# Optimization experiments

Measured on AMD Instinct MI355X. Metric: run time of the kernel, lower is better.

The kernel has to match this reference:

```python
import jax, jax.numpy as jnp
import numpy as np

NEG_SLOPE_GAT = 0.2    # PyG GATConv default negative_slope
NEG_SLOPE_ACT = 0.01   # F.leaky_relu default
D_DIRECTIONS = 4       # len(target): message directions per variable (uniform in this setup)
GAT_HEADS = 4


def gru_cell(x, h, Wih, Whh, bih, bhh):
    # torch.nn.GRUCell math; Wih [3H, in], Whh [3H, H]
    gi = x @ Wih.T + bih
    gh = h @ Whh.T + bhh
    ir, iz, inn = jnp.split(gi, 3, axis=1)
    hr, hz, hn = jnp.split(gh, 3, axis=1)
    r = jax.nn.sigmoid(ir + hr)
    z = jax.nn.sigmoid(iz + hz)
    n = jnp.tanh(inn + r * hn)
    return (1.0 - z) * n + z * h


def gat_conv(x, W, a_src, a_dst, bias, src, dst, heads, concat):
    # PyG GATConv (self-loops already included in src/dst)
    N = x.shape[0]
    C = W.shape[1] // heads
    h = (x @ W).reshape(N, heads, C)
    as_ = jnp.einsum('nhc,hc->nh', h, a_src)
    ad = jnp.einsum('nhc,hc->nh', h, a_dst)
    e = jax.nn.leaky_relu(as_[src] + ad[dst], NEG_SLOPE_GAT)  # [E, heads]
    m = jax.ops.segment_max(e, dst, num_segments=N)
    ex = jnp.exp(e - m[dst])
    den = jax.ops.segment_sum(ex, dst, num_segments=N)
    alpha = ex / den[dst]
    out = jax.ops.segment_sum(h[src] * alpha[:, :, None], dst, num_segments=N)
    if concat:
        return out.reshape(N, heads * C) + bias
    return out.mean(axis=1) + bias


def setup_inputs():
    key = jax.random.key(0)
    ki = iter(jax.random.split(key, 64))
    nk = lambda: next(ki)
    Nx, A, B = 100000, 50000, 50000
    IC, PD = 16, 3
    GH = IC - PD  # gru hidden = 13
    E, M, G, L, H, OC = 2000000, 1024, 1024, 4, 4, 32
    Ntot = Nx + A + B

    def p(*shape):
        return jax.random.normal(nk(), shape, jnp.float32) * 0.05

    inp = {}
    inp['x'] = jax.random.normal(nk(), (Nx, IC), jnp.float32)
    inp['edge_index'] = jax.random.randint(nk(), (2, E), 0, Ntot)
    inp['ass_to_sum_msg'] = jax.random.normal(nk(), (A, 1), jnp.float32)
    inp['ass_to_sum_hidden'] = jax.random.normal(nk(), (A, GH), jnp.float32)
    inp['sum_to_ass_msg'] = jax.random.normal(nk(), (B, 1), jnp.float32)
    inp['sum_to_ass_hidden'] = jax.random.normal(nk(), (B, GH), jnp.float32)
    inp['prefix'] = jax.random.normal(nk(), (A + B, PD), jnp.float32)
    inp['function_node_idxes'] = jax.random.randint(nk(), (M,), 0, Ntot)
    # regularized neighbor_idx_info: group g has direction idx=group_idx[g], src list group_src[g]
    # with idx at position 0 (out_i == 0) and no other entry equal to idx.
    gidx = jax.random.randint(nk(), (G,), 0, M)
    gs = jax.random.randint(nk(), (G, L), 0, M)
    rest = jnp.where(gs[:, 1:] == gidx[:, None], (gidx[:, None] + 1) % M, gs[:, 1:])
    inp['group_idx'] = gidx
    inp['group_src'] = jnp.concatenate([gidx[:, None], rest], axis=1)
    # GRU params
    for g in ('gru1', 'gru2'):
        inp[g + '_Wih'] = p(3 * GH, 1)
        inp[g + '_Whh'] = p(3 * GH, GH)
        inp[g + '_bih'] = p(3 * GH)
        inp[g + '_bhh'] = p(3 * GH)
    # GATConv params (W stored [in, heads*out], used as x @ W)
    inp['W1'] = p(IC, 32); inp['asrc1'] = p(4, 8); inp['adst1'] = p(4, 8); inp['b1'] = p(32)
    inp['W2'] = p(32, 32); inp['asrc2'] = p(4, 8); inp['adst2'] = p(4, 8); inp['b2'] = p(32)
    inp['W3'] = p(32, 32); inp['asrc3'] = p(4, 8); inp['adst3'] = p(4, 8); inp['b3'] = p(32)
    inp['W4'] = p(32, 4 * OC); inp['asrc4'] = p(4, OC); inp['adst4'] = p(4, OC); inp['b4'] = p(OC)
    # Attention heads: Wq/Wk [H, OC, OC] (applied as v @ Wq[h]), Ws [H, 2*OC], bs [H]
    inp['Wq'] = p(H, OC, OC); inp['Wk'] = p(H, OC, OC); inp['Ws'] = p(H, 2 * OC); inp['bs'] = p(H)
    return inp


def reference(x, edge_index, ass_to_sum_msg, ass_to_sum_hidden, sum_to_ass_msg,
              sum_to_ass_hidden, prefix, function_node_idxes, group_idx, group_src,
              gru1_Wih, gru1_Whh, gru1_bih, gru1_bhh,
              gru2_Wih, gru2_Whh, gru2_bih, gru2_bhh,
              W1, asrc1, adst1, b1, W2, asrc2, adst2, b2,
              W3, asrc3, adst3, b3, W4, asrc4, adst4, b4,
              Wq, Wk, Ws, bs):
    h1 = gru_cell(ass_to_sum_msg, ass_to_sum_hidden, gru1_Wih, gru1_Whh, gru1_bih, gru1_bhh)
    h2 = gru_cell(sum_to_ass_msg, sum_to_ass_hidden, gru2_Wih, gru2_Whh, gru2_bih, gru2_bhh)
    hidden = jnp.concatenate([h1, h2], axis=0)
    hidden = jnp.concatenate([prefix, hidden], axis=1)
    xx = jnp.concatenate([x, hidden], axis=0)
    N = xx.shape[0]
    loop = jnp.arange(N)
    src = jnp.concatenate([edge_index[0], loop])  # add self loops (PyG default)
    dst = jnp.concatenate([edge_index[1], loop])
    xx = jax.nn.leaky_relu(gat_conv(xx, W1, asrc1, adst1, b1, src, dst, GAT_HEADS, True), NEG_SLOPE_ACT)
    xx = jax.nn.leaky_relu(gat_conv(xx, W2, asrc2, adst2, b2, src, dst, GAT_HEADS, True), NEG_SLOPE_ACT)
    xx = jax.nn.leaky_relu(gat_conv(xx, W3, asrc3, adst3, b3, src, dst, GAT_HEADS, True), NEG_SLOPE_ACT)
    xx = jax.nn.leaky_relu(gat_conv(xx, W4, asrc4, adst4, b4, src, dst, GAT_HEADS, False), NEG_SLOPE_ACT)
    pooling = xx[function_node_idxes]  # [M, OC]
    hdim = pooling.shape[1]
    # score(i,j,h) = sigmoid((pooling_i @ Wq_h) . ws_q_h + (pooling_j @ Wk_h) . ws_k_h + bs_h)
    # (associativity: equals sigmoid(score_proj(cat([q_proj, k_proj]))) of the original)
    Vq = jnp.einsum('hdo,ho->hd', Wq, Ws[:, :hdim])
    Vk = jnp.einsum('hdo,ho->hd', Wk, Ws[:, hdim:])
    sq = pooling @ Vq.T  # [M, H]
    sk = pooling @ Vk.T  # [M, H]
    scores = jax.nn.sigmoid(sq[:, None, :] + sk[None, :, :] + bs)  # [M, M, H]; flat n -> (n//M, n%M)
    idx = group_idx
    nbr = group_src[:, 1:]  # idx itself sits at position 0 and is removed
    gathered = scores[idx[:, None], nbr]  # [G, L-1, H]
    trg = scores[idx, idx]                # [G, H]
    score_sum = gathered.mean(axis=1)
    tw = jax.nn.softmax(jnp.stack([score_sum, trg], axis=0), axis=0)  # [2, G, H]
    w = jax.nn.softmax(gathered, axis=1) * tw[0][:, None, :] * (D_DIRECTIONS - 1)
    weights = jnp.concatenate([tw[1][:, None, :], w], axis=1)  # [G, L, H] (out_i == 0)
    return weights, h1, h2
```

## Files before the change

### kernel.cpp

```cpp
#include <hip/hip_runtime.h>
#include <hip/hip_bf16.h>

#define NXD   100000
#define AROWS 50000
#define NND   200000
#define EED   2000000
#define ETOT  2200000
#define GHD   13
#define MMD   1024

#define OUT_H1 16384
#define OUT_H2 (16384 + AROWS * GHD)

#define NB    196
#define BSH   10
#define CAP   16000
#define TILE  4096

typedef __hip_bfloat16 bf16;
typedef unsigned int uvec4 __attribute__((ext_vector_type(4)));

__device__ __forceinline__ float bf2f(bf16 v) { return __bfloat162float(v); }
__device__ __forceinline__ float sigm(float x) { return 1.f / (1.f + __expf(-x)); }
__device__ __forceinline__ float tanhfast(float x) {
    x = fminf(15.f, fmaxf(-15.f, x));
    float t = __expf(-2.f * x);
    return (1.f - t) / (1.f + t);
}
__device__ __forceinline__ float lrelu(float x, float s) { return x > 0.f ? x : s * x; }

__device__ __forceinline__ unsigned short f2bf_bits(float v) {
    bf16 b = __float2bfloat16(v);
    return *reinterpret_cast<unsigned short*>(&b);
}
__device__ __forceinline__ float bflo(unsigned int u) { return __uint_as_float((u & 0xFFFFu) << 16); }
__device__ __forceinline__ float bfhi(unsigned int u) { return __uint_as_float(u & 0xFFFF0000u); }

__device__ __forceinline__ float loadF(const void* p, size_t i, int f32) {
    return f32 ? ((const float*)p)[i] : bf2f(((const bf16*)p)[i]);
}
__device__ __forceinline__ void storeF(void* p, size_t i, float v, int f32) {
    if (f32) ((float*)p)[i] = v;
    else ((bf16*)p)[i] = __float2bfloat16(v);
}

__global__ void detect_kernel(const void* __restrict__ xp, int* __restrict__ flag,
                              int* __restrict__ gtail) {
    int lane = threadIdx.x;
    const unsigned short* u = (const unsigned short*)xp;
    unsigned short b = u[lane * 2];
    int e = (b >> 7) & 0xFF;
    int viol = (e == 0xFF) || (e < 64) || (e > 190);
    unsigned long long mask = __ballot(viol != 0);
    if (lane == 0) flag[0] = (__popcll(mask) > 8) ? 1 : 0;
    for (int i = lane; i < NB; i += 64) gtail[i] = 0;
}

__global__ void assemble_kernel(const void* __restrict__ x, const void* __restrict__ prefix,
                                bf16* __restrict__ bufA, const int* __restrict__ flag) {
    int f = *flag;
    int t = blockIdx.x * 256 + threadIdx.x;
    if (t < NXD * 16) {
        bufA[t] = __float2bfloat16(loadF(x, t, f));
    } else {
        int u = t - NXD * 16;
        if (u < NXD * 3) {
            int r = u / 3, c = u - r * 3;
            bufA[(size_t)(NXD + r) * 16 + c] = __float2bfloat16(loadF(prefix, u, f));
        }
    }
}

__global__ void gru2_kernel(const void* __restrict__ msg1, const void* __restrict__ hid1,
                            const void* __restrict__ Wih1, const void* __restrict__ Whh1,
                            const void* __restrict__ bih1, const void* __restrict__ bhh1,
                            const void* __restrict__ msg2, const void* __restrict__ hid2,
                            const void* __restrict__ Wih2, const void* __restrict__ Whh2,
                            const void* __restrict__ bih2, const void* __restrict__ bhh2,
                            void* __restrict__ dout, bf16* __restrict__ xxA,
                            const int* __restrict__ flag) {
    int f = *flag;
    int which = blockIdx.x >= 196;
    const void* msg = which ? msg2 : msg1;
    const void* hid = which ? hid2 : hid1;
    const void* Wih = which ? Wih2 : Wih1;
    const void* Whh = which ? Whh2 : Whh1;
    const void* bih = which ? bih2 : bih1;
    const void* bhh = which ? bhh2 : bhh1;
    size_t houtbase = which ? (size_t)OUT_H2 : (size_t)OUT_H1;
    int rowbase = which ? AROWS : 0;
    int blk = blockIdx.x - (which ? 196 : 0);
    __shared__ float WhhL[39 * 13], WihL[39], bihL[39], bhhL[39];
    int tid = threadIdx.x;
    for (int i = tid; i < 39 * 13; i += 256) WhhL[i] = loadF(Whh, i, f);
    if (tid < 39) { WihL[tid] = loadF(Wih, tid, f); bihL[tid] = loadF(bih, tid, f); bhhL[tid] = loadF(bhh, tid, f); }
    __syncthreads();
    int n = blk * 256 + tid;
    if (n >= AROWS) return;
    float x = loadF(msg, n, f);
    float h[GHD];
#pragma unroll
    for (int k = 0; k < GHD; k++) h[k] = loadF(hid, n * GHD + k, f);
#pragma unroll
    for (int k = 0; k < GHD; k++) {
        float gir = fmaf(x, WihL[k],      bihL[k]);
        float giz = fmaf(x, WihL[13 + k], bihL[13 + k]);
        float gin = fmaf(x, WihL[26 + k], bihL[26 + k]);
        float ghr = bhhL[k], ghz = bhhL[13 + k], ghn = bhhL[26 + k];
#pragma unroll
        for (int q = 0; q < GHD; q++) {
            ghr = fmaf(h[q], WhhL[k * 13 + q],        ghr);
            ghz = fmaf(h[q], WhhL[(13 + k) * 13 + q], ghz);
            ghn = fmaf(h[q], WhhL[(26 + k) * 13 + q], ghn);
        }
        float r = sigm(gir + ghr);
        float z = sigm(giz + ghz);
        float nn = tanhfast(gin + r * ghn);
        float o = (1.f - z) * nn + z * h[k];
        storeF(dout, houtbase + (size_t)n * GHD + k, o, f);
        xxA[(size_t)(NXD + rowbase + n) * 16 + 3 + k] = __float2bfloat16(o);
    }
}

__global__ void bin_kernel(const int* __restrict__ src_e, const int* __restrict__ dst_e,
                           int* __restrict__ gtail, unsigned int* __restrict__ stage) {
    __shared__ int hist[NB];
    __shared__ int base[NB];
    __shared__ int cur[NB];
    int tid = threadIdx.x;
    for (int i = tid; i < NB; i += 256) hist[i] = 0;
    __syncthreads();
    int t0 = blockIdx.x * TILE;
    int tend = t0 + TILE; if (tend > ETOT) tend = ETOT;
    for (int t = t0 + tid; t < tend; t += 256) {
        int d = (t < EED) ? dst_e[t] : (t - EED);
        atomicAdd(&hist[d >> BSH], 1);
    }
    __syncthreads();
    for (int i = tid; i < NB; i += 256) {
        int c = hist[i];
        base[i] = (c > 0) ? atomicAdd(&gtail[i], c) : 0;
        cur[i] = 0;
    }
    __syncthreads();
    for (int t = t0 + tid; t < tend; t += 256) {
        int s, d;
        if (t < EED) { s = src_e[t]; d = dst_e[t]; } else { s = d = t - EED; }
        int b = d >> BSH;
        int p = base[b] + atomicAdd(&cur[b], 1);
        if (p < CAP)
            stage[(size_t)b * CAP + p] = ((unsigned int)(d & 1023) << 18) | (unsigned int)s;
    }
}

__global__ void build_kernel(const unsigned int* __restrict__ stage,
                             const int* __restrict__ gtail,
                             int* __restrict__ offs, int* __restrict__ csr) {
    __shared__ int cnt[1024];
    __shared__ int loc[1024];
    __shared__ int cur[1024];
    __shared__ int lds[256];
    int b = blockIdx.x;
    int tid = threadIdx.x;
    int v = (tid < NB) ? gtail[tid] : 0;
    lds[tid] = v; __syncthreads();
    for (int off = 1; off < 256; off <<= 1) {
        int t2 = (tid >= off) ? lds[tid - off] : 0;
        __syncthreads();
        lds[tid] += t2;
        __syncthreads();
    }
    __shared__ int ebs;
    if (tid == b) ebs = lds[tid] - v;
    __syncthreads();
    int eb = ebs;
    int nE = gtail[b]; if (nE > CAP) nE = CAP;
    const unsigned int* st = stage + (size_t)b * CAP;
    for (int i = tid; i < 1024; i += 256) cnt[i] = 0;
    __syncthreads();
    for (int i = tid; i < nE; i += 256)
        atomicAdd(&cnt[st[i] >> 18], 1);
    __syncthreads();
    int c0 = cnt[tid * 4], c1 = cnt[tid * 4 + 1], c2 = cnt[tid * 4 + 2], c3 = cnt[tid * 4 + 3];
    int s = c0 + c1 + c2 + c3;
    lds[tid] = s; __syncthreads();
    for (int off = 1; off < 256; off <<= 1) {
        int t2 = (tid >= off) ? lds[tid - off] : 0;
        __syncthreads();
        lds[tid] += t2;
        __syncthreads();
    }
    int run = lds[tid] - s;
    loc[tid * 4]     = run;
    loc[tid * 4 + 1] = run + c0;
    loc[tid * 4 + 2] = run + c0 + c1;
    loc[tid * 4 + 3] = run + c0 + c1 + c2;
    __syncthreads();
    int nodebase = b << BSH;
    for (int i = tid; i < 1024; i += 256) {
        cur[i] = loc[i];
        int n = nodebase + i;
        if (n < NND) offs[n] = eb + loc[i];
    }
    if (b == 0 && tid == 0) offs[NND] = ETOT;
    __syncthreads();
    for (int i = tid; i < nE; i += 256) {
        unsigned int e = st[i];
        int dl = e >> 18;
        int src = e & 0x3FFFF;
        int p = atomicAdd(&cur[dl], 1);
        csr[eb + p] = src;
    }
}

template <int K>
__global__ void feat_kernel(const bf16* __restrict__ xx,
                            const void* __restrict__ W,
                            bf16* __restrict__ hbuf, const int* __restrict__ flag) {
    int f = *flag;
    int tid = threadIdx.x;
    int j = tid & 31;
    float Wc[K];
#pragma unroll
    for (int k = 0; k < K; k++) Wc[k] = loadF(W, k * 32 + j, f);
    int half = blockIdx.x * 8 + (tid >> 5);
    if (half >= NND / 16) return;
    int n0 = half * 16;
#pragma unroll 4
    for (int n = n0; n < n0 + 16; n++) {
        const uvec4* xr4 = (const uvec4*)(xx + (size_t)n * K);
        float v = 0.f;
#pragma unroll
        for (int q = 0; q < K / 8; q++) {
            uvec4 u = xr4[q];
            v = fmaf(bflo(u.x), Wc[q * 8 + 0], v);
            v = fmaf(bfhi(u.x), Wc[q * 8 + 1], v);
            v = fmaf(bflo(u.y), Wc[q * 8 + 2], v);
            v = fmaf(bfhi(u.y), Wc[q * 8 + 3], v);
            v = fmaf(bflo(u.z), Wc[q * 8 + 4], v);
            v = fmaf(bfhi(u.z), Wc[q * 8 + 5], v);
            v = fmaf(bflo(u.w), Wc[q * 8 + 6], v);
            v = fmaf(bfhi(u.w), Wc[q * 8 + 7], v);
        }
        hbuf[(size_t)n * 32 + j] = __float2bfloat16(v);
    }
}

__global__ void agg_kernel(const bf16* __restrict__ hbuf, const int* __restrict__ offs,
                           const int* __restrict__ csr, const void* __restrict__ asrc,
                           const void* __restrict__ adst, const void* __restrict__ bias,
                           bf16* __restrict__ xxout, const int* __restrict__ flag) {
    int f = *flag;
    __shared__ float bl[32], asl[32], adl[32];
    int tid = threadIdx.x;
    if (tid < 32) {
        bl[tid]  = loadF(bias, tid, f);
        asl[tid] = loadF(asrc, tid, f);
        adl[tid] = loadF(adst, tid, f);
    }
    __syncthreads();
    int n = blockIdx.x * 64 + (tid >> 2);
    int j = tid & 3;
    int cb = 8 * j;
    float A0 = asl[cb], A1 = asl[cb + 1], A2 = asl[cb + 2], A3 = asl[cb + 3];
    float A4 = asl[cb + 4], A5 = asl[cb + 5], A6 = asl[cb + 6], A7 = asl[cb + 7];
    uvec4 hd = *(const uvec4*)(hbuf + (size_t)n * 32 + cb);
    float adv = bflo(hd.x) * adl[cb]     + bfhi(hd.x) * adl[cb + 1]
              + bflo(hd.y) * adl[cb + 2] + bfhi(hd.y) * adl[cb + 3]
              + bflo(hd.z) * adl[cb + 4] + bfhi(hd.z) * adl[cb + 5]
              + bflo(hd.w) * adl[cb + 6] + bfhi(hd.w) * adl[cb + 7];
    int beg = offs[n], end = offs[n + 1];
    int cnt = end - beg;
    const int* cp = csr + beg;
    int s0 = cp[0];
    uvec4 h0 = *(const uvec4*)(hbuf + (size_t)s0 * 32 + cb);
    uvec4 h1 = h0;
    if (cnt > 1) {
        int s1 = cp[1];
        h1 = *(const uvec4*)(hbuf + (size_t)s1 * 32 + cb);
    }
    float den = 0.f;
    float a0 = 0.f, a1 = 0.f, a2 = 0.f, a3 = 0.f, a4 = 0.f, a5 = 0.f, a6 = 0.f, a7 = 0.f;
    for (int i = 0; i < cnt; i++) {
        uvec4 hn = (uvec4)(0u);
        if (i + 2 < cnt) {
            int sn = cp[i + 2];
            hn = *(const uvec4*)(hbuf + (size_t)sn * 32 + cb);
        }
        float v0 = bflo(h0.x), v1 = bfhi(h0.x), v2 = bflo(h0.y), v3 = bfhi(h0.y);
        float v4 = bflo(h0.z), v5 = bfhi(h0.z), v6 = bflo(h0.w), v7 = bfhi(h0.w);
        float as = v0 * A0 + v1 * A1 + v2 * A2 + v3 * A3
                 + v4 * A4 + v5 * A5 + v6 * A6 + v7 * A7;
        float e = as + adv;
        e = e > 0.f ? e : 0.2f * e;
        e = fminf(50.f, fmaxf(-50.f, e));
        float w = __expf(e);
        den += w;
        a0 = fmaf(w, v0, a0); a1 = fmaf(w, v1, a1);
        a2 = fmaf(w, v2, a2); a3 = fmaf(w, v3, a3);
        a4 = fmaf(w, v4, a4); a5 = fmaf(w, v5, a5);
        a6 = fmaf(w, v6, a6); a7 = fmaf(w, v7, a7);
        h0 = h1; h1 = hn;
    }
    float inv = 1.f / den;
    float o0 = lrelu(fmaf(a0, inv, bl[cb + 0]), 0.01f);
    float o1 = lrelu(fmaf(a1, inv, bl[cb + 1]), 0.01f);
    float o2 = lrelu(fmaf(a2, inv, bl[cb + 2]), 0.01f);
    float o3 = lrelu(fmaf(a3, inv, bl[cb + 3]), 0.01f);
    float o4 = lrelu(fmaf(a4, inv, bl[cb + 4]), 0.01f);
    float o5 = lrelu(fmaf(a5, inv, bl[cb + 5]), 0.01f);
    float o6 = lrelu(fmaf(a6, inv, bl[cb + 6]), 0.01f);
    float o7 = lrelu(fmaf(a7, inv, bl[cb + 7]), 0.01f);
    uvec4 p;
    p.x = ((unsigned int)f2bf_bits(o1) << 16) | f2bf_bits(o0);
    p.y = ((unsigned int)f2bf_bits(o3) << 16) | f2bf_bits(o2);
    p.z = ((unsigned int)f2bf_bits(o5) << 16) | f2bf_bits(o4);
    p.w = ((unsigned int)f2bf_bits(o7) << 16) | f2bf_bits(o6);
    __builtin_nontemporal_store(p, (uvec4*)(xxout + (size_t)n * 32 + cb));
}

__global__ void layer4_kernel(const bf16* __restrict__ xx,
                              const void* __restrict__ W4,
                              const void* __restrict__ asrc,
                              const void* __restrict__ adst,
                              const void* __restrict__ b4,
                              const int* __restrict__ fidx, const int* __restrict__ offs,
                              const int* __restrict__ csr, float* __restrict__ pool,
                              const int* __restrict__ flag) {
    int f = *flag;
    __shared__ float Wl[32 * 128];
    __shared__ float asl[128], adl[128], bl[32];
    __shared__ float accs[4][32];
    __shared__ float dens[4];
    int tid = threadIdx.x;
    for (int i = tid; i < 32 * 128; i += 256) Wl[i] = loadF(W4, i, f);
    if (tid < 128) { asl[tid] = loadF(asrc, tid, f); adl[tid] = loadF(adst, tid, f); accs[tid >> 5][tid & 31] = 0.f; }
    if (tid < 32) bl[tid] = loadF(b4, tid, f);
    if (tid < 4) dens[tid] = 0.f;
    __syncthreads();
    int g = blockIdx.x;
    int d = fidx[g];
    int wave = tid >> 6, lane = tid & 63;
    int c = lane & 31;
    int h0 = lane >> 5;
    int h1 = h0 + 2;
    const uvec4* xd4 = (const uvec4*)(xx + (size_t)d * 32);
    uvec4 du0 = xd4[0], du1 = xd4[1];
    float v0 = 0.f, v1 = 0.f;
    {
        unsigned int us[8] = {du0.x, du0.y, du0.z, du0.w, du1.x, du1.y, du1.z, du1.w};
#pragma unroll
        for (int q = 0; q < 8; q++) {
            unsigned int u = us[q];
            int k = 2 * q;
            v0 = fmaf(bflo(u), Wl[k * 128 + lane], v0);       v0 = fmaf(bfhi(u), Wl[(k + 1) * 128 + lane], v0);
            v1 = fmaf(bflo(u), Wl[k * 128 + lane + 64], v1);  v1 = fmaf(bfhi(u), Wl[(k + 1) * 128 + lane + 64], v1);
        }
    }
    float ad0 = v0 * adl[h0 * 32 + c];
    float ad1 = v1 * adl[h1 * 32 + c];
#pragma unroll
    for (int mk = 1; mk < 32; mk <<= 1) { ad0 += __shfl_xor(ad0, mk); ad1 += __shfl_xor(ad1, mk); }
    int beg = offs[d], end = offs[d + 1];
    float den0 = 0.f, den1 = 0.f, acc0 = 0.f, acc1 = 0.f;
    for (int i = beg + wave; i < end; i += 4) {
        int s = csr[i];
        const uvec4* xs4 = (const uvec4*)(xx + (size_t)s * 32);
        uvec4 su0 = xs4[0], su1 = xs4[1];
        float s0 = 0.f, s1 = 0.f;
        unsigned int us[8] = {su0.x, su0.y, su0.z, su0.w, su1.x, su1.y, su1.z, su1.w};
#pragma unroll
        for (int q = 0; q < 8; q++) {
            unsigned int u = us[q];
            int k = 2 * q;
            s0 = fmaf(bflo(u), Wl[k * 128 + lane], s0);       s0 = fmaf(bfhi(u), Wl[(k + 1) * 128 + lane], s0);
            s1 = fmaf(bflo(u), Wl[k * 128 + lane + 64], s1);  s1 = fmaf(bfhi(u), Wl[(k + 1) * 128 + lane + 64], s1);
        }
        float as0 = s0 * asl[h0 * 32 + c];
        float as1 = s1 * asl[h1 * 32 + c];
#pragma unroll
        for (int mk = 1; mk < 32; mk <<= 1) { as0 += __shfl_xor(as0, mk); as1 += __shfl_xor(as1, mk); }
        float e0 = lrelu(as0 + ad0, 0.2f);
        float e1 = lrelu(as1 + ad1, 0.2f);
        e0 = fminf(50.f, fmaxf(-50.f, e0));
        e1 = fminf(50.f, fmaxf(-50.f, e1));
        float w0 = __expf(e0), w1 = __expf(e1);
        den0 += w0; acc0 = fmaf(w0, s0, acc0);
        den1 += w1; acc1 = fmaf(w1, s1, acc1);
    }
    atomicAdd(&accs[h0][c], acc0);
    atomicAdd(&accs[h1][c], acc1);
    if (c == 0) { atomicAdd(&dens[h0], den0); atomicAdd(&dens[h1], den1); }
    __syncthreads();
    if (tid < 32) {
        float t = accs[0][tid] / dens[0] + accs[1][tid] / dens[1]
                + accs[2][tid] / dens[2] + accs[3][tid] / dens[3];
        float o = t * 0.25f + bl[tid];
        pool[g * 32 + tid] = lrelu(o, 0.01f);
    }
}

__global__ void tail_kernel(const void* __restrict__ Wq, const void* __restrict__ Wk,
                            const void* __restrict__ Ws, const void* __restrict__ bs,
                            const int* __restrict__ gidx, const int* __restrict__ gsrc,
                            const float* __restrict__ pool, void* __restrict__ out,
                            const int* __restrict__ flag) {
    int f = *flag;
    __shared__ float vq[128], vk[128];
    __shared__ float sq[4096], sk[4096];
    int tid = threadIdx.x;
    {
        int which = tid >> 7;
        int i = tid & 127;
        int h = i >> 5, dd = i & 31;
        const void* Wm = which ? Wk : Wq;
        float sum = 0.f;
#pragma unroll
        for (int o = 0; o < 32; o++)
            sum = fmaf(loadF(Wm, (h * 32 + dd) * 32 + o, f), loadF(Ws, h * 64 + which * 32 + o, f), sum);
        (which ? vk : vq)[i] = sum;
    }
    __syncthreads();
    for (int idx = tid; idx < 8192; idx += 256) {
        int which = idx >> 12;
        int i = idx & 4095;
        int g = i >> 2, h = i & 3;
        const float* V = which ? vk : vq;
        float s = 0.f;
#pragma unroll
        for (int dd = 0; dd < 32; dd++) s = fmaf(pool[g * 32 + dd], V[h * 32 + dd], s);
        (which ? sk : sq)[i] = s;
    }
    __syncthreads();
    for (int t = tid; t < 4096; t += 256) {
        int g = t >> 2, h = t & 3;
        int i = gidx[g];
        float bsv = loadF(bs, h, f);
        float sqi = sq[i * 4 + h];
        float trg = sigm(sqi + sk[i * 4 + h] + bsv);
        float ga[3];
#pragma unroll
        for (int q = 0; q < 3; q++) {
            int jj = gsrc[g * 4 + 1 + q];
            ga[q] = sigm(sqi + sk[jj * 4 + h] + bsv);
        }
        float ss = (ga[0] + ga[1] + ga[2]) * (1.f / 3.f);
        float mx = fmaxf(ss, trg);
        float e0 = __expf(ss - mx), e1 = __expf(trg - mx);
        float inv = 1.f / (e0 + e1);
        float tw0 = e0 * inv, tw1 = e1 * inv;
        float mg = fmaxf(ga[0], fmaxf(ga[1], ga[2]));
        float w0 = __expf(ga[0] - mg), w1 = __expf(ga[1] - mg), w2 = __expf(ga[2] - mg);
        float wi = tw0 * 3.f / (w0 + w1 + w2);
        storeF(out, g * 16 + 0 + h,  tw1,     f);
        storeF(out, g * 16 + 4 + h,  w0 * wi, f);
        storeF(out, g * 16 + 8 + h,  w1 * wi, f);
        storeF(out, g * 16 + 12 + h, w2 * wi, f);
    }
}

extern "C" void kernel_launch(void* const* d_in, const int* in_sizes, int n_in,
                              void* d_out, int out_size, void* d_ws, size_t ws_size,
                              hipStream_t stream) {
    const void* x        = d_in[0];
    const int*  ei       = (const int*)d_in[1];
    const void* a2s_msg  = d_in[2];
    const void* a2s_hid  = d_in[3];
    const void* s2a_msg  = d_in[4];
    const void* s2a_hid  = d_in[5];
    const void* prefix   = d_in[6];
    const int*  fidx     = (const int*)d_in[7];
    const int*  gidx     = (const int*)d_in[8];
    const int*  gsrc     = (const int*)d_in[9];
    const void* g1_Wih   = d_in[10];
    const void* g1_Whh   = d_in[11];
    const void* g1_bih   = d_in[12];
    const void* g1_bhh   = d_in[13];
    const void* g2_Wih   = d_in[14];
    const void* g2_Whh   = d_in[15];
    const void* g2_bih   = d_in[16];
    const void* g2_bhh   = d_in[17];
    const void* W1  = d_in[18];
    const void* as1 = d_in[19];
    const void* ad1 = d_in[20];
    const void* b1  = d_in[21];
    const void* W2  = d_in[22];
    const void* as2 = d_in[23];
    const void* ad2 = d_in[24];
    const void* b2  = d_in[25];
    const void* W3  = d_in[26];
    const void* as3 = d_in[27];
    const void* ad3 = d_in[28];
    const void* b3  = d_in[29];
    const void* W4  = d_in[30];
    const void* as4 = d_in[31];
    const void* ad4 = d_in[32];
    const void* b4  = d_in[33];
    const void* Wq  = d_in[34];
    const void* Wk  = d_in[35];
    const void* Ws  = d_in[36];
    const void* bs  = d_in[37];

    const int* src_e = ei;
    const int* dst_e = ei + EED;

    char* wp = (char*)d_ws;
    auto alloc = [&](size_t bytes) {
        char* p = wp;
        wp += (bytes + 255) & ~(size_t)255;
        return p;
    };
    int*   csr   = (int*)alloc((size_t)ETOT * 4);
    int*   offs  = (int*)alloc((size_t)(NND + 1) * 4);
    int*   gtail = (int*)alloc((size_t)NB * 4);
    int*   dflag = (int*)alloc(256);
    float* pool  = (float*)alloc((size_t)MMD * 32 * 4);
    bf16*  bufA  = (bf16*)alloc((size_t)NND * 32 * 2);
    bf16*  bufB  = (bf16*)alloc((size_t)NND * 32 * 2);
    unsigned int* stage = (unsigned int*)bufB;

    detect_kernel<<<1, 64, 0, stream>>>(x, dflag, gtail);

    assemble_kernel<<<(NXD * 19 + 255) / 256, 256, 0, stream>>>(x, prefix, bufA, dflag);
    gru2_kernel<<<392, 256, 0, stream>>>(a2s_msg, a2s_hid, g1_Wih, g1_Whh, g1_bih, g1_bhh,
                                         s2a_msg, s2a_hid, g2_Wih, g2_Whh, g2_bih, g2_bhh,
                                         d_out, bufA, dflag);

    bin_kernel<<<(ETOT + TILE - 1) / TILE, 256, 0, stream>>>(src_e, dst_e, gtail, stage);
    build_kernel<<<NB, 256, 0, stream>>>(stage, gtail, offs, csr);

    const int nblk_feat = (NND / 16 + 7) / 8;
    const int nblk_agg  = NND / 64;
    feat_kernel<16><<<nblk_feat, 256, 0, stream>>>(bufA, W1, bufB, dflag);
    agg_kernel<<<nblk_agg, 256, 0, stream>>>(bufB, offs, csr, as1, ad1, b1, bufA, dflag);
    feat_kernel<32><<<nblk_feat, 256, 0, stream>>>(bufA, W2, bufB, dflag);
    agg_kernel<<<nblk_agg, 256, 0, stream>>>(bufB, offs, csr, as2, ad2, b2, bufA, dflag);
    feat_kernel<32><<<nblk_feat, 256, 0, stream>>>(bufA, W3, bufB, dflag);
    agg_kernel<<<nblk_agg, 256, 0, stream>>>(bufB, offs, csr, as3, ad3, b3, bufA, dflag);

    layer4_kernel<<<MMD, 256, 0, stream>>>(bufA, W4, as4, ad4, b4, fidx, offs, csr, pool, dflag);

    tail_kernel<<<1, 256, 0, stream>>>(Wq, Wk, Ws, bs, gidx, gsrc, pool, d_out, dflag);
}
```

Measured before the change: 454.4 us.

## Fuse prep stages into one launch, degree-sort agg nodes, deepen prefetch

Merges the edge binning, input assembly and the two GRU cells into a single prep kernel, and runs CSR build alongside the first feature transform in one mid kernel. A separate stage buffer allows that overlap. The dtype flag is now recomputed in every block instead of being read from a detect kernel's output. A per-bin degree-sorted node order is built so agg warps handle nodes of similar degree, and the agg gather prefetch goes from two rows ahead to three. This cuts launch count and serial gaps, at the cost of an extra indirection, an extra buffer, and per-block flag detection.

```diff
diff --git a/kernel.cpp b/kernel.cpp
--- a/kernel.cpp
+++ b/kernel.cpp
@@ -17,6 +17,11 @@
 #define CAP   16000
 #define TILE  4096
 
+#define PREP_BIN   538
+#define PREP_ASM   7422
+#define PREP_GRU   392
+#define FEAT_BLK   1563
+
 typedef __hip_bfloat16 bf16;
 typedef unsigned int uvec4 __attribute__((ext_vector_type(4)));
 
@@ -44,186 +49,125 @@
     else ((bf16*)p)[i] = __float2bfloat16(v);
 }
 
-__global__ void detect_kernel(const void* __restrict__ xp, int* __restrict__ flag,
-                              int* __restrict__ gtail) {
-    int lane = threadIdx.x;
-    const unsigned short* u = (const unsigned short*)xp;
-    unsigned short b = u[lane * 2];
-    int e = (b >> 7) & 0xFF;
-    int viol = (e == 0xFF) || (e < 64) || (e > 190);
-    unsigned long long mask = __ballot(viol != 0);
-    if (lane == 0) flag[0] = (__popcll(mask) > 8) ? 1 : 0;
-    for (int i = lane; i < NB; i += 64) gtail[i] = 0;
-}
-
-__global__ void assemble_kernel(const void* __restrict__ x, const void* __restrict__ prefix,
-                                bf16* __restrict__ bufA, const int* __restrict__ flag) {
-    int f = *flag;
-    int t = blockIdx.x * 256 + threadIdx.x;
-    if (t < NXD * 16) {
-        bufA[t] = __float2bfloat16(loadF(x, t, f));
-    } else {
-        int u = t - NXD * 16;
-        if (u < NXD * 3) {
-            int r = u / 3, c = u - r * 3;
-            bufA[(size_t)(NXD + r) * 16 + c] = __float2bfloat16(loadF(prefix, u, f));
-        }
-    }
-}
-
-__global__ void gru2_kernel(const void* __restrict__ msg1, const void* __restrict__ hid1,
+__device__ __forceinline__ int flag_from_x(const void* xp, int tid, int* fl) {
+    if (tid < 64) {
+        const unsigned short* u = (const unsigned short*)xp;
+        unsigned short b = u[tid * 2];
+        int e = (b >> 7) & 0xFF;
+        int viol = (e == 0xFF) || (e < 64) || (e > 190);
+        unsigned long long mask = __ballot(viol != 0);
+        if (tid == 0) *fl = (__popcll(mask) > 8) ? 1 : 0;
+    }
+    __syncthreads();
+    return *fl;
+}
+
+__global__ void prep_kernel(const void* __restrict__ x, const void* __restrict__ prefix,
+                            const void* __restrict__ msg1, const void* __restrict__ hid1,
                             const void* __restrict__ Wih1, const void* __restrict__ Whh1,
                             const void* __restrict__ bih1, const void* __restrict__ bhh1,
                             const void* __restrict__ msg2, const void* __restrict__ hid2,
                             const void* __restrict__ Wih2, const void* __restrict__ Whh2,
                             const void* __restrict__ bih2, const void* __restrict__ bhh2,
-                            void* __restrict__ dout, bf16* __restrict__ xxA,
-                            const int* __restrict__ flag) {
-    int f = *flag;
-    int which = blockIdx.x >= 196;
-    const void* msg = which ? msg2 : msg1;
-    const void* hid = which ? hid2 : hid1;
-    const void* Wih = which ? Wih2 : Wih1;
-    const void* Whh = which ? Whh2 : Whh1;
-    const void* bih = which ? bih2 : bih1;
-    const void* bhh = which ? bhh2 : bhh1;
-    size_t houtbase = which ? (size_t)OUT_H2 : (size_t)OUT_H1;
-    int rowbase = which ? AROWS : 0;
-    int blk = blockIdx.x - (which ? 196 : 0);
-    __shared__ float WhhL[39 * 13], WihL[39], bihL[39], bhhL[39];
-    int tid = threadIdx.x;
-    for (int i = tid; i < 39 * 13; i += 256) WhhL[i] = loadF(Whh, i, f);
-    if (tid < 39) { WihL[tid] = loadF(Wih, tid, f); bihL[tid] = loadF(bih, tid, f); bhhL[tid] = loadF(bhh, tid, f); }
-    __syncthreads();
-    int n = blk * 256 + tid;
-    if (n >= AROWS) return;
-    float x = loadF(msg, n, f);
-    float h[GHD];
-#pragma unroll
-    for (int k = 0; k < GHD; k++) h[k] = loadF(hid, n * GHD + k, f);
-#pragma unroll
-    for (int k = 0; k < GHD; k++) {
-        float gir = fmaf(x, WihL[k],      bihL[k]);
-        float giz = fmaf(x, WihL[13 + k], bihL[13 + k]);
-        float gin = fmaf(x, WihL[26 + k], bihL[26 + k]);
-        float ghr = bhhL[k], ghz = bhhL[13 + k], ghn = bhhL[26 + k];
-#pragma unroll
-        for (int q = 0; q < GHD; q++) {
-            ghr = fmaf(h[q], WhhL[k * 13 + q],        ghr);
-            ghz = fmaf(h[q], WhhL[(13 + k) * 13 + q], ghz);
-            ghn = fmaf(h[q], WhhL[(26 + k) * 13 + q], ghn);
-        }
-        float r = sigm(gir + ghr);
-        float z = sigm(giz + ghz);
-        float nn = tanhfast(gin + r * ghn);
-        float o = (1.f - z) * nn + z * h[k];
-        storeF(dout, houtbase + (size_t)n * GHD + k, o, f);
-        xxA[(size_t)(NXD + rowbase + n) * 16 + 3 + k] = __float2bfloat16(o);
-    }
-}
-
-__global__ void bin_kernel(const int* __restrict__ src_e, const int* __restrict__ dst_e,
-                           int* __restrict__ gtail, unsigned int* __restrict__ stage) {
+                            void* __restrict__ dout, bf16* __restrict__ bufA,
+                            const int* __restrict__ src_e, const int* __restrict__ dst_e,
+                            int* __restrict__ gtail, unsigned int* __restrict__ stage) {
     __shared__ int hist[NB];
     __shared__ int base[NB];
     __shared__ int cur[NB];
-    int tid = threadIdx.x;
-    for (int i = tid; i < NB; i += 256) hist[i] = 0;
-    __syncthreads();
-    int t0 = blockIdx.x * TILE;
-    int tend = t0 + TILE; if (tend > ETOT) tend = ETOT;
-    for (int t = t0 + tid; t < tend; t += 256) {
-        int d = (t < EED) ? dst_e[t] : (t - EED);
-        atomicAdd(&hist[d >> BSH], 1);
-    }
-    __syncthreads();
-    for (int i = tid; i < NB; i += 256) {
-        int c = hist[i];
-        base[i] = (c > 0) ? atomicAdd(&gtail[i], c) : 0;
-        cur[i] = 0;
-    }
-    __syncthreads();
-    for (int t = t0 + tid; t < tend; t += 256) {
-        int s, d;
-        if (t < EED) { s = src_e[t]; d = dst_e[t]; } else { s = d = t - EED; }
-        int b = d >> BSH;
-        int p = base[b] + atomicAdd(&cur[b], 1);
-        if (p < CAP)
-            stage[(size_t)b * CAP + p] = ((unsigned int)(d & 1023) << 18) | (unsigned int)s;
-    }
-}
-
-__global__ void build_kernel(const unsigned int* __restrict__ stage,
-                             const int* __restrict__ gtail,
-                             int* __restrict__ offs, int* __restrict__ csr) {
-    __shared__ int cnt[1024];
-    __shared__ int loc[1024];
-    __shared__ int cur[1024];
-    __shared__ int lds[256];
-    int b = blockIdx.x;
-    int tid = threadIdx.x;
-    int v = (tid < NB) ? gtail[tid] : 0;
-    lds[tid] = v; __syncthreads();
-    for (int off = 1; off < 256; off <<= 1) {
-        int t2 = (tid >= off) ? lds[tid - off] : 0;
-        __syncthreads();
-        lds[tid] += t2;
-        __syncthreads();
-    }
-    __shared__ int ebs;
-    if (tid == b) ebs = lds[tid] - v;
-    __syncthreads();
-    int eb = ebs;
-    int nE = gtail[b]; if (nE > CAP) nE = CAP;
-    const unsigned int* st = stage + (size_t)b * CAP;
-    for (int i = tid; i < 1024; i += 256) cnt[i] = 0;
-    __syncthreads();
-    for (int i = tid; i < nE; i += 256)
-        atomicAdd(&cnt[st[i] >> 18], 1);
-    __syncthreads();
-    int c0 = cnt[tid * 4], c1 = cnt[tid * 4 + 1], c2 = cnt[tid * 4 + 2], c3 = cnt[tid * 4 + 3];
-    int s = c0 + c1 + c2 + c3;
-    lds[tid] = s; __syncthreads();
-    for (int off = 1; off < 256; off <<= 1) {
-        int t2 = (tid >= off) ? lds[tid - off] : 0;
-        __syncthreads();
-        lds[tid] += t2;
-        __syncthreads();
-    }
-    int run = lds[tid] - s;
-    loc[tid * 4]     = run;
-    loc[tid * 4 + 1] = run + c0;
-    loc[tid * 4 + 2] = run + c0 + c1;
-    loc[tid * 4 + 3] = run + c0 + c1 + c2;
-    __syncthreads();
-    int nodebase = b << BSH;
-    for (int i = tid; i < 1024; i += 256) {
-        cur[i] = loc[i];
-        int n = nodebase + i;
-        if (n < NND) offs[n] = eb + loc[i];
-    }
-    if (b == 0 && tid == 0) offs[NND] = ETOT;
-    __syncthreads();
-    for (int i = tid; i < nE; i += 256) {
-        unsigned int e = st[i];
-        int dl = e >> 18;
-        int src = e & 0x3FFFF;
-        int p = atomicAdd(&cur[dl], 1);
-        csr[eb + p] = src;
+    __shared__ float WhhL[39 * 13], WihL[39], bihL[39], bhhL[39];
+    __shared__ int fl;
+    int bid = blockIdx.x, tid = threadIdx.x;
+    if (bid < PREP_BIN) {
+        for (int i = tid; i < NB; i += 256) hist[i] = 0;
+        __syncthreads();
+        int t0 = bid * TILE;
+        int tend = t0 + TILE; if (tend > ETOT) tend = ETOT;
+        for (int t = t0 + tid; t < tend; t += 256) {
+            int d = (t < EED) ? dst_e[t] : (t - EED);
+            atomicAdd(&hist[d >> BSH], 1);
+        }
+        __syncthreads();
+        for (int i = tid; i < NB; i += 256) {
+            int c = hist[i];
+            base[i] = (c > 0) ? atomicAdd(&gtail[i], c) : 0;
+            cur[i] = 0;
+        }
+        __syncthreads();
+        for (int t = t0 + tid; t < tend; t += 256) {
+            int s, d;
+            if (t < EED) { s = src_e[t]; d = dst_e[t]; } else { s = d = t - EED; }
+            int b = d >> BSH;
+            int p = base[b] + atomicAdd(&cur[b], 1);
+            if (p < CAP)
+                stage[(size_t)b * CAP + p] = ((unsigned int)(d & 1023) << 18) | (unsigned int)s;
+        }
+    } else if (bid < PREP_BIN + PREP_ASM) {
+        int f = flag_from_x(x, tid, &fl);
+        int t = (bid - PREP_BIN) * 256 + tid;
+        if (t < NXD * 16) {
+            bufA[t] = __float2bfloat16(loadF(x, t, f));
+        } else {
+            int u = t - NXD * 16;
+            if (u < NXD * 3) {
+                int r = u / 3, c = u - r * 3;
+                bufA[(size_t)(NXD + r) * 16 + c] = __float2bfloat16(loadF(prefix, u, f));
+            }
+        }
+    } else {
+        int f = flag_from_x(x, tid, &fl);
+        int vb = bid - PREP_BIN - PREP_ASM;
+        int which = vb >= 196;
+        const void* msg = which ? msg2 : msg1;
+        const void* hid = which ? hid2 : hid1;
+        const void* Wih = which ? Wih2 : Wih1;
+        const void* Whh = which ? Whh2 : Whh1;
+        const void* bih = which ? bih2 : bih1;
+        const void* bhh = which ? bhh2 : bhh1;
+        size_t houtbase = which ? (size_t)OUT_H2 : (size_t)OUT_H1;
+        int rowbase = which ? AROWS : 0;
+        int blk = vb - (which ? 196 : 0);
+        for (int i = tid; i < 39 * 13; i += 256) WhhL[i] = loadF(Whh, i, f);
+        if (tid < 39) { WihL[tid] = loadF(Wih, tid, f); bihL[tid] = loadF(bih, tid, f); bhhL[tid] = loadF(bhh, tid, f); }
+        __syncthreads();
+        int n = blk * 256 + tid;
+        if (n >= AROWS) return;
+        float xv = loadF(msg, n, f);
+        float h[GHD];
+#pragma unroll
+        for (int k = 0; k < GHD; k++) h[k] = loadF(hid, n * GHD + k, f);
+#pragma unroll
+        for (int k = 0; k < GHD; k++) {
+            float gir = fmaf(xv, WihL[k],      bihL[k]);
+            float giz = fmaf(xv, WihL[13 + k], bihL[13 + k]);
+            float gin = fmaf(xv, WihL[26 + k], bihL[26 + k]);
+            float ghr = bhhL[k], ghz = bhhL[13 + k], ghn = bhhL[26 + k];
+#pragma unroll
+            for (int q = 0; q < GHD; q++) {
+                ghr = fmaf(h[q], WhhL[k * 13 + q],        ghr);
+                ghz = fmaf(h[q], WhhL[(13 + k) * 13 + q], ghz);
+                ghn = fmaf(h[q], WhhL[(26 + k) * 13 + q], ghn);
+            }
+            float r = sigm(gir + ghr);
+            float z = sigm(giz + ghz);
+            float nn = tanhfast(gin + r * ghn);
+            float o = (1.f - z) * nn + z * h[k];
+            storeF(dout, houtbase + (size_t)n * GHD + k, o, f);
+            bufA[(size_t)(NXD + rowbase + n) * 16 + 3 + k] = __float2bfloat16(o);
+        }
     }
 }
 
 template <int K>
-__global__ void feat_kernel(const bf16* __restrict__ xx,
-                            const void* __restrict__ W,
-                            bf16* __restrict__ hbuf, const int* __restrict__ flag) {
-    int f = *flag;
-    int tid = threadIdx.x;
+__device__ __forceinline__ void feat_body(const bf16* __restrict__ xx,
+                                          const void* __restrict__ W,
+                                          bf16* __restrict__ hbuf, int f,
+                                          int vbid, int tid) {
     int j = tid & 31;
     float Wc[K];
 #pragma unroll
     for (int k = 0; k < K; k++) Wc[k] = loadF(W, k * 32 + j, f);
-    int half = blockIdx.x * 8 + (tid >> 5);
+    int half = vbid * 8 + (tid >> 5);
     if (half >= NND / 16) return;
     int n0 = half * 16;
 #pragma unroll 4
@@ -246,20 +190,116 @@
     }
 }
 
+__global__ void mid_kernel(const unsigned int* __restrict__ stage, const int* __restrict__ gtail,
+                           int* __restrict__ offs, int* __restrict__ csr, int* __restrict__ order,
+                           const bf16* __restrict__ xx, const void* __restrict__ W,
+                           bf16* __restrict__ hbuf, const void* __restrict__ x) {
+    __shared__ int cnt[1024];
+    __shared__ int loc[1024];
+    __shared__ int cur[1024];
+    __shared__ int lds[256];
+    __shared__ int dh[64];
+    __shared__ int fl;
+    int bid = blockIdx.x, tid = threadIdx.x;
+    if (bid >= NB) {
+        int f = flag_from_x(x, tid, &fl);
+        feat_body<16>(xx, W, hbuf, f, bid - NB, tid);
+        return;
+    }
+    int b = bid;
+    int v = (tid < NB) ? gtail[tid] : 0;
+    lds[tid] = v; __syncthreads();
+    for (int off = 1; off < 256; off <<= 1) {
+        int t2 = (tid >= off) ? lds[tid - off] : 0;
+        __syncthreads();
+        lds[tid] += t2;
+        __syncthreads();
+    }
+    __shared__ int ebs;
+    if (tid == b) ebs = lds[tid] - v;
+    __syncthreads();
+    int eb = ebs;
+    int nE = gtail[b]; if (nE > CAP) nE = CAP;
+    const unsigned int* st = stage + (size_t)b * CAP;
+    for (int i = tid; i < 1024; i += 256) cnt[i] = 0;
+    __syncthreads();
+    for (int i = tid; i < nE; i += 256)
+        atomicAdd(&cnt[st[i] >> 18], 1);
+    __syncthreads();
+    int c0 = cnt[tid * 4], c1 = cnt[tid * 4 + 1], c2 = cnt[tid * 4 + 2], c3 = cnt[tid * 4 + 3];
+    int s = c0 + c1 + c2 + c3;
+    lds[tid] = s; __syncthreads();
+    for (int off = 1; off < 256; off <<= 1) {
+        int t2 = (tid >= off) ? lds[tid - off] : 0;
+        __syncthreads();
+        lds[tid] += t2;
+        __syncthreads();
+    }
+    int run = lds[tid] - s;
+    loc[tid * 4]     = run;
+    loc[tid * 4 + 1] = run + c0;
+    loc[tid * 4 + 2] = run + c0 + c1;
+    loc[tid * 4 + 3] = run + c0 + c1 + c2;
+    __syncthreads();
+    int nodebase = b << BSH;
+    int bcnt = NND - nodebase; if (bcnt > 1024) bcnt = 1024;
+    for (int i = tid; i < 1024; i += 256) {
+        cur[i] = loc[i];
+        int n = nodebase + i;
+        if (n < NND) offs[n] = eb + loc[i];
+    }
+    if (b == 0 && tid == 0) offs[NND] = ETOT;
+    if (tid < 64) dh[tid] = 0;
+    __syncthreads();
+    for (int i = tid; i < nE; i += 256) {
+        unsigned int e = st[i];
+        int dl = e >> 18;
+        int src = e & 0x3FFFF;
+        int p = atomicAdd(&cur[dl], 1);
+        csr[eb + p] = src;
+    }
+    for (int i = tid; i < bcnt; i += 256) {
+        int dcl = cnt[i]; if (dcl > 63) dcl = 63;
+        atomicAdd(&dh[dcl], 1);
+    }
+    __syncthreads();
+    if (tid == 0) {
+        int acc = 0;
+        for (int k = 0; k < 64; k++) { int c = dh[k]; dh[k] = acc; acc += c; }
+    }
+    __syncthreads();
+    for (int i = tid; i < bcnt; i += 256) {
+        int dcl = cnt[i]; if (dcl > 63) dcl = 63;
+        int pos = atomicAdd(&dh[dcl], 1);
+        order[nodebase + pos] = nodebase + i;
+    }
+}
+
+template <int K>
+__global__ void feat_kernel(const bf16* __restrict__ xx, const void* __restrict__ W,
+                            bf16* __restrict__ hbuf, const void* __restrict__ x) {
+    __shared__ int fl;
+    int tid = threadIdx.x;
+    int f = flag_from_x(x, tid, &fl);
+    feat_body<K>(xx, W, hbuf, f, blockIdx.x, tid);
+}
+
 __global__ void agg_kernel(const bf16* __restrict__ hbuf, const int* __restrict__ offs,
-                           const int* __restrict__ csr, const void* __restrict__ asrc,
-                           const void* __restrict__ adst, const void* __restrict__ bias,
-                           bf16* __restrict__ xxout, const int* __restrict__ flag) {
-    int f = *flag;
+                           const int* __restrict__ csr, const int* __restrict__ order,
+                           const void* __restrict__ asrc, const void* __restrict__ adst,
+                           const void* __restrict__ bias, bf16* __restrict__ xxout,
+                           const void* __restrict__ x) {
     __shared__ float bl[32], asl[32], adl[32];
+    __shared__ int fl;
     int tid = threadIdx.x;
+    int f = flag_from_x(x, tid, &fl);
     if (tid < 32) {
         bl[tid]  = loadF(bias, tid, f);
         asl[tid] = loadF(asrc, tid, f);
         adl[tid] = loadF(adst, tid, f);
     }
     __syncthreads();
-    int n = blockIdx.x * 64 + (tid >> 2);
+    int n = order[blockIdx.x * 64 + (tid >> 2)];
     int j = tid & 3;
     int cb = 8 * j;
     float A0 = asl[cb], A1 = asl[cb + 1], A2 = asl[cb + 2], A3 = asl[cb + 3];
@@ -272,19 +312,16 @@
     int beg = offs[n], end = offs[n + 1];
     int cnt = end - beg;
     const int* cp = csr + beg;
-    int s0 = cp[0];
-    uvec4 h0 = *(const uvec4*)(hbuf + (size_t)s0 * 32 + cb);
-    uvec4 h1 = h0;
-    if (cnt > 1) {
-        int s1 = cp[1];
-        h1 = *(const uvec4*)(hbuf + (size_t)s1 * 32 + cb);
-    }
+    uvec4 h0 = *(const uvec4*)(hbuf + (size_t)cp[0] * 32 + cb);
+    uvec4 h1 = h0, h2 = h0;
+    if (cnt > 1) h1 = *(const uvec4*)(hbuf + (size_t)cp[1] * 32 + cb);
+    if (cnt > 2) h2 = *(const uvec4*)(hbuf + (size_t)cp[2] * 32 + cb);
     float den = 0.f;
     float a0 = 0.f, a1 = 0.f, a2 = 0.f, a3 = 0.f, a4 = 0.f, a5 = 0.f, a6 = 0.f, a7 = 0.f;
     for (int i = 0; i < cnt; i++) {
         uvec4 hn = (uvec4)(0u);
-        if (i + 2 < cnt) {
-            int sn = cp[i + 2];
+        if (i + 3 < cnt) {
+            int sn = cp[i + 3];
             hn = *(const uvec4*)(hbuf + (size_t)sn * 32 + cb);
         }
         float v0 = bflo(h0.x), v1 = bfhi(h0.x), v2 = bflo(h0.y), v3 = bfhi(h0.y);
@@ -300,7 +337,7 @@
         a2 = fmaf(w, v2, a2); a3 = fmaf(w, v3, a3);
         a4 = fmaf(w, v4, a4); a5 = fmaf(w, v5, a5);
         a6 = fmaf(w, v6, a6); a7 = fmaf(w, v7, a7);
-        h0 = h1; h1 = hn;
+        h0 = h1; h1 = h2; h2 = hn;
     }
     float inv = 1.f / den;
     float o0 = lrelu(fmaf(a0, inv, bl[cb + 0]), 0.01f);
@@ -326,13 +363,14 @@
                               const void* __restrict__ b4,
                               const int* __restrict__ fidx, const int* __restrict__ offs,
                               const int* __restrict__ csr, float* __restrict__ pool,
-                              const int* __restrict__ flag) {
-    int f = *flag;
+                              const void* __restrict__ x) {
     __shared__ float Wl[32 * 128];
     __shared__ float asl[128], adl[128], bl[32];
     __shared__ float accs[4][32];
     __shared__ float dens[4];
+    __shared__ int fl;
     int tid = threadIdx.x;
+    int f = flag_from_x(x, tid, &fl);
     for (int i = tid; i < 32 * 128; i += 256) Wl[i] = loadF(W4, i, f);
     if (tid < 128) { asl[tid] = loadF(asrc, tid, f); adl[tid] = loadF(adst, tid, f); accs[tid >> 5][tid & 31] = 0.f; }
     if (tid < 32) bl[tid] = loadF(b4, tid, f);
@@ -404,11 +442,12 @@
                             const void* __restrict__ Ws, const void* __restrict__ bs,
                             const int* __restrict__ gidx, const int* __restrict__ gsrc,
                             const float* __restrict__ pool, void* __restrict__ out,
-                            const int* __restrict__ flag) {
-    int f = *flag;
+                            const void* __restrict__ x) {
     __shared__ float vq[128], vk[128];
     __shared__ float sq[4096], sk[4096];
+    __shared__ int fl;
     int tid = threadIdx.x;
+    int f = flag_from_x(x, tid, &fl);
     {
         int which = tid >> 7;
         int i = tid & 127;
@@ -512,33 +551,30 @@
     };
     int*   csr   = (int*)alloc((size_t)ETOT * 4);
     int*   offs  = (int*)alloc((size_t)(NND + 1) * 4);
+    int*   order = (int*)alloc((size_t)NND * 4);
     int*   gtail = (int*)alloc((size_t)NB * 4);
-    int*   dflag = (int*)alloc(256);
     float* pool  = (float*)alloc((size_t)MMD * 32 * 4);
     bf16*  bufA  = (bf16*)alloc((size_t)NND * 32 * 2);
     bf16*  bufB  = (bf16*)alloc((size_t)NND * 32 * 2);
-    unsigned int* stage = (unsigned int*)bufB;
-
-    detect_kernel<<<1, 64, 0, stream>>>(x, dflag, gtail);
-
-    assemble_kernel<<<(NXD * 19 + 255) / 256, 256, 0, stream>>>(x, prefix, bufA, dflag);
-    gru2_kernel<<<392, 256, 0, stream>>>(a2s_msg, a2s_hid, g1_Wih, g1_Whh, g1_bih, g1_bhh,
-                                         s2a_msg, s2a_hid, g2_Wih, g2_Whh, g2_bih, g2_bhh,
-                                         d_out, bufA, dflag);
-
-    bin_kernel<<<(ETOT + TILE - 1) / TILE, 256, 0, stream>>>(src_e, dst_e, gtail, stage);
-    build_kernel<<<NB, 256, 0, stream>>>(stage, gtail, offs, csr);
-
-    const int nblk_feat = (NND / 16 + 7) / 8;
-    const int nblk_agg  = NND / 64;
-    feat_kernel<16><<<nblk_feat, 256, 0, stream>>>(bufA, W1, bufB, dflag);
-    agg_kernel<<<nblk_agg, 256, 0, stream>>>(bufB, offs, csr, as1, ad1, b1, bufA, dflag);
-    feat_kernel<32><<<nblk_feat, 256, 0, stream>>>(bufA, W2, bufB, dflag);
-    agg_kernel<<<nblk_agg, 256, 0, stream>>>(bufB, offs, csr, as2, ad2, b2, bufA, dflag);
-    feat_kernel<32><<<nblk_feat, 256, 0, stream>>>(bufA, W3, bufB, dflag);
-    agg_kernel<<<nblk_agg, 256, 0, stream>>>(bufB, offs, csr, as3, ad3, b3, bufA, dflag);
-
-    layer4_kernel<<<MMD, 256, 0, stream>>>(bufA, W4, as4, ad4, b4, fidx, offs, csr, pool, dflag);
-
-    tail_kernel<<<1, 256, 0, stream>>>(Wq, Wk, Ws, bs, gidx, gsrc, pool, d_out, dflag);
-}
+    unsigned int* stage = (unsigned int*)alloc((size_t)NB * CAP * 4);
+
+    hipMemsetAsync(gtail, 0, (size_t)NB * 4, stream);
+    prep_kernel<<<PREP_BIN + PREP_ASM + PREP_GRU, 256, 0, stream>>>(
+        x, prefix,
+        a2s_msg, a2s_hid, g1_Wih, g1_Whh, g1_bih, g1_bhh,
+        s2a_msg, s2a_hid, g2_Wih, g2_Whh, g2_bih, g2_bhh,
+        d_out, bufA, src_e, dst_e, gtail, stage);
+
+    mid_kernel<<<NB + FEAT_BLK, 256, 0, stream>>>(stage, gtail, offs, csr, order,
+                                                  bufA, W1, bufB, x);
+
+    const int nblk_agg = NND / 64;
+    agg_kernel<<<nblk_agg, 256, 0, stream>>>(bufB, offs, csr, order, as1, ad1, b1, bufA, x);
+    feat_kernel<32><<<FEAT_BLK, 256, 0, stream>>>(bufA, W2, bufB, x);
+    agg_kernel<<<nblk_agg, 256, 0, stream>>>(bufB, offs, csr, order, as2, ad2, b2, bufA, x);
+    feat_kernel<32><<<FEAT_BLK, 256, 0, stream>>>(bufA, W3, bufB, x);
+    agg_kernel<<<nblk_agg, 256, 0, stream>>>(bufB, offs, csr, order, as3, ad3, b3, bufA, x);
+
+    layer4_kernel<<<MMD, 256, 0, stream>>>(bufA, W4, as4, ad4, b4, fidx, offs, csr, pool, x);
+    tail_kernel<<<1, 256, 0, stream>>>(Wq, Wk, Ws, bs, gidx, gsrc, pool, d_out, x);
+}
```

Measured after the change: 496.9 us. 1.09x slower.
